# Performance work log

Measured on AMD Instinct MI355X. Metric: run time of the kernel, lower is better.

Reference implementation:

```python
import jax, jax.numpy as jnp
import numpy as np

N_NODES = 50000

def _gcn_conv(x, W, b, src, dst, num_nodes):
    # PyG GCNConv: linear transform, then D^{-1/2} A_hat D^{-1/2} aggregation (A_hat has self-loops).
    xw = x @ W                                   # [N, out]
    ones = jnp.ones(src.shape[0], dtype=x.dtype)
    deg = jax.ops.segment_sum(ones, dst, num_segments=num_nodes)  # in-degree incl. self loop
    dinv = jnp.where(deg > 0, jax.lax.rsqrt(deg), 0.0)
    norm = dinv[src] * dinv[dst]                 # [E]
    msg = xw[src] * norm[:, None]                # [E, out] gather + scale
    out = jax.ops.segment_sum(msg, dst, num_segments=num_nodes)   # scatter-add
    return out + b

def _add_self_loops(edge_index, num_nodes):
    loop = jnp.arange(num_nodes, dtype=edge_index.dtype)
    src = jnp.concatenate([edge_index[0], loop])
    dst = jnp.concatenate([edge_index[1], loop])
    return src, dst

def setup_inputs() -> dict:
    key = jax.random.key(0)
    k = jax.random.split(key, 6)
    in_dim, hid_dim, out_dim = 256, 128, 64
    n_edges = 800000
    x = jax.random.normal(k[0], (N_NODES, in_dim), dtype=jnp.float32)
    edge_index = jax.random.randint(k[1], (2, n_edges), 0, N_NODES, dtype=jnp.int64)
    W1 = jax.random.normal(k[2], (in_dim, hid_dim), dtype=jnp.float32) / np.sqrt(in_dim)
    b1 = jnp.zeros((hid_dim,), dtype=jnp.float32)
    W2 = jax.random.normal(k[3], (hid_dim, out_dim), dtype=jnp.float32) / np.sqrt(hid_dim)
    b2 = jnp.zeros((out_dim,), dtype=jnp.float32)
    return {"x": x, "edge_index": edge_index, "W1": W1, "b1": b1, "W2": W2, "b2": b2}

def reference(x, edge_index, W1, b1, W2, b2):
    src, dst = _add_self_loops(edge_index, N_NODES)
    h = jnp.tanh(_gcn_conv(x, W1, b1, src, dst, N_NODES))
    out = _gcn_conv(h, W2, b2, src, dst, N_NODES)
    return out
```

## Files before the change

### kernel.cpp

```cpp
#include <hip/hip_runtime.h>

#define INDIM 256
#define HID 128
#define OUTD 64
#define BINSHIFT 8
#define MAXBIN 256

typedef _Float16 f16x8 __attribute__((ext_vector_type(8)));
typedef float    f32x4 __attribute__((ext_vector_type(4)));

__global__ __launch_bounds__(256) void k_hist_setup(const int* __restrict__ dst, int* __restrict__ bin_counts,
                                                    int E,
                                                    const float* __restrict__ W1, const float* __restrict__ W2,
                                                    _Float16* __restrict__ W1t, _Float16* __restrict__ W2t) {
    __shared__ int h[MAXBIN];
    int tid = threadIdx.x;
    h[tid] = 0;
    __syncthreads();
    int base = blockIdx.x * 4096;
#pragma unroll
    for (int i = 0; i < 16; i++) {
        int e = base + i * 256 + tid;
        if (e < E) atomicAdd(&h[dst[e] >> BINSHIFT], 1);
    }
    __syncthreads();
    int v = h[tid];
    if (v) atomicAdd(&bin_counts[tid], v);

    constexpr int NW1 = HID * INDIM;
    constexpr int NW2 = OUTD * HID;
    int id = blockIdx.x * 256 + tid;
    if (id < NW1) {
        int n = id / INDIM, k = id % INDIM;
        W1t[id] = (_Float16)W1[k * HID + n];
    } else if (id < NW1 + NW2) {
        int j = id - NW1;
        int n = j / HID, k = j % HID;
        W2t[j] = (_Float16)W2[k * OUTD + n];
    }
}

struct __align__(16) GemmSh { _Float16 As[128][40]; _Float16 Bs[128][40]; };
struct FillSh { int h[256]; int s[256]; int rb[256]; };
struct CsrSh  { int A[256]; int B[256]; int C[256]; };
union FillU { FillSh f; GemmSh g; };
union CsrU  { CsrSh  c; GemmSh g; };

template <int BN, int K, typename AT>
__device__ __forceinline__ void gemm_body(const AT* __restrict__ X, const _Float16* __restrict__ Wt,
                                          _Float16* __restrict__ XW, int M, int rb,
                                          _Float16 (*As)[40], _Float16 (*Bs)[40])
{
    constexpr int NT = BN / 16;
    const int tid  = threadIdx.x;
    const int wave = tid >> 6;
    const int lane = tid & 63;
    const int m    = lane & 15;
    const int q    = lane >> 4;

    f32x4 acc[2][NT];
#pragma unroll
    for (int r = 0; r < 2; r++)
#pragma unroll
        for (int t = 0; t < NT; t++) acc[r][t] = (f32x4){0.f, 0.f, 0.f, 0.f};

    for (int kt = 0; kt < K; kt += 32) {
        if (kt) __syncthreads();
        if constexpr (sizeof(AT) == 4) {
#pragma unroll
            for (int i = 0; i < 4; i++) {
                int ch = tid + i * 256;
                int row = ch >> 3, c4 = ch & 7, gr = rb + row;
                float4 v = make_float4(0.f, 0.f, 0.f, 0.f);
                if (gr < M) v = *(const float4*)((const float*)X + (long)gr * K + kt + c4 * 4);
                _Float16* p = &As[row][c4 * 4];
                p[0] = (_Float16)v.x; p[1] = (_Float16)v.y;
                p[2] = (_Float16)v.z; p[3] = (_Float16)v.w;
            }
        } else {
#pragma unroll
            for (int i = 0; i < 2; i++) {
                int ch = tid + i * 256;
                int row = ch >> 2, c8 = ch & 3, gr = rb + row;
                uint4 v = make_uint4(0u, 0u, 0u, 0u);
                if (gr < M) v = *(const uint4*)((const _Float16*)X + (long)gr * K + kt + c8 * 8);
                *(uint4*)(&As[row][c8 * 8]) = v;
            }
        }
#pragma unroll
        for (int i = 0; i < BN / 64; i++) {
            int ch = tid + i * 256;
            int n = ch >> 2, c8 = ch & 3;
            *(uint4*)(&Bs[n][c8 * 8]) = *(const uint4*)(Wt + (long)n * K + kt + c8 * 8);
        }
        __syncthreads();

        f16x8 a0 = *(const f16x8*)(&As[wave * 32 + m][q * 8]);
        f16x8 a1 = *(const f16x8*)(&As[wave * 32 + 16 + m][q * 8]);
#pragma unroll
        for (int t = 0; t < NT; t++) {
            f16x8 bf = *(const f16x8*)(&Bs[t * 16 + m][q * 8]);
            acc[0][t] = __builtin_amdgcn_mfma_f32_16x16x32_f16(a0, bf, acc[0][t], 0, 0, 0);
            acc[1][t] = __builtin_amdgcn_mfma_f32_16x16x32_f16(a1, bf, acc[1][t], 0, 0, 0);
        }
    }

#pragma unroll
    for (int r2 = 0; r2 < 2; r2++) {
        int row0 = rb + wave * 32 + r2 * 16 + q * 4;
#pragma unroll
        for (int rr = 0; rr < 4; rr++) {
            int row = row0 + rr;
            if (row < M) {
#pragma unroll
                for (int t = 0; t < NT; t++)
                    XW[(long)row * BN + t * 16 + m] = (_Float16)acc[r2][t][rr];
            }
        }
    }
}

__device__ __forceinline__ void fill_body(const int* __restrict__ src, const int* __restrict__ dst,
                                          const int* __restrict__ bin_counts, int* __restrict__ bin_cursor,
                                          int* __restrict__ binned, int E, FillSh& sh)
{
    int tid = threadIdx.x;
    sh.h[tid] = 0;
    int v = bin_counts[tid];
    sh.s[tid] = v;
    __syncthreads();
    int base = blockIdx.x * 2048;
    int ep[8], eb[8], rk[8];
#pragma unroll
    for (int i = 0; i < 8; i++) {
        int e = base + i * 256 + tid;
        if (e < E) {
            int s = src[e], d = dst[e];
            ep[i] = (s << 8) | (d & 255);
            eb[i] = d >> BINSHIFT;
            rk[i] = atomicAdd(&sh.h[eb[i]], 1);
        } else {
            eb[i] = -1;
        }
    }
#pragma unroll
    for (int off = 1; off < 256; off <<= 1) {
        int t = (tid >= off) ? sh.s[tid - off] : 0;
        __syncthreads();
        sh.s[tid] += t;
        __syncthreads();
    }
    int c = sh.h[tid];
    if (c) sh.rb[tid] = (sh.s[tid] - v) + atomicAdd(&bin_cursor[tid], c);
    __syncthreads();
#pragma unroll
    for (int i = 0; i < 8; i++) {
        if (eb[i] >= 0) binned[sh.rb[eb[i]] + rk[i]] = ep[i];
    }
}

__device__ __forceinline__ void csr_body(const int* __restrict__ binned, const int* __restrict__ bin_counts,
                                         int* __restrict__ row_start, float* __restrict__ dinv,
                                         int* __restrict__ edge_src, int M, int E, CsrSh& sh)
{
    int b = blockIdx.x, tid = threadIdx.x;
    int v = bin_counts[tid];
    sh.A[tid] = v;
    __syncthreads();
#pragma unroll
    for (int off = 1; off < 256; off <<= 1) {
        int t = (tid >= off) ? sh.A[tid - off] : 0;
        __syncthreads();
        sh.A[tid] += t;
        __syncthreads();
    }
    sh.B[tid] = sh.A[tid] - v;
    __syncthreads();
    int beg = sh.B[b];
    int end = (b + 1 < 256) ? sh.B[b + 1] : E;
    if (b == 0 && tid == 0) row_start[M] = E;

    sh.A[tid] = 0;
    __syncthreads();
    for (int i = beg + tid; i < end; i += 256) {
        atomicAdd(&sh.A[binned[i] & 255], 1);
    }
    __syncthreads();
    int c = sh.A[tid];
    sh.B[tid] = c;
    __syncthreads();
#pragma unroll
    for (int off = 1; off < 256; off <<= 1) {
        int t = (tid >= off) ? sh.B[tid - off] : 0;
        __syncthreads();
        sh.B[tid] += t;
        __syncthreads();
    }
    int start = beg + sh.B[tid] - c;
    int node = (b << BINSHIFT) + tid;
    if (node < M) {
        row_start[node] = start;
        dinv[node] = rsqrtf(1.0f + (float)c);
    }
    sh.C[tid] = start;
    __syncthreads();
    for (int i = beg + tid; i < end; i += 256) {
        int p = binned[i];
        int pos = atomicAdd(&sh.C[p & 255], 1);
        edge_src[pos] = p >> 8;
    }
}

__global__ __launch_bounds__(256) void k_binfill_gemm(
    const int* __restrict__ src, const int* __restrict__ dst,
    const int* __restrict__ bin_counts, int* __restrict__ bin_cursor, int* __restrict__ binned, int E,
    const float* __restrict__ X, const _Float16* __restrict__ W1t, _Float16* __restrict__ XW, int M,
    int nfill, int rbofs)
{
    __shared__ FillU u;
    if ((int)blockIdx.x < nfill)
        fill_body(src, dst, bin_counts, bin_cursor, binned, E, u.f);
    else
        gemm_body<HID, INDIM, float>(X, W1t, XW, M, (rbofs + (int)blockIdx.x - nfill) * 128, u.g.As, u.g.Bs);
}

__global__ __launch_bounds__(256) void k_csr_gemm(
    const int* __restrict__ binned, const int* __restrict__ bin_counts,
    int* __restrict__ row_start, float* __restrict__ dinv, int* __restrict__ edge_src, int M, int E,
    const float* __restrict__ X, const _Float16* __restrict__ W1t, _Float16* __restrict__ XW,
    int nbin, int rbofs)
{
    __shared__ CsrU u;
    if ((int)blockIdx.x < nbin)
        csr_body(binned, bin_counts, row_start, dinv, edge_src, M, E, u.c);
    else
        gemm_body<HID, INDIM, float>(X, W1t, XW, M, (rbofs + (int)blockIdx.x - nbin) * 128, u.g.As, u.g.Bs);
}

template <int BN, int K, typename AT>
__global__ __launch_bounds__(256) void k_gemm_mfma(const AT* __restrict__ X, const _Float16* __restrict__ Wt,
                                                   _Float16* __restrict__ XW, int M)
{
    __shared__ __align__(16) _Float16 As[128][40];
    __shared__ __align__(16) _Float16 Bs[BN][40];
    gemm_body<BN, K, AT>(X, Wt, XW, M, (int)blockIdx.x * 128, As, Bs);
}

template <int F, bool TANH, typename OutT>
__global__ __launch_bounds__(256) void k_agg_csr(const int* __restrict__ row_start,
                                                 const int* __restrict__ edge_src,
                                                 const _Float16* __restrict__ feat,
                                                 const float* __restrict__ bias,
                                                 const float* __restrict__ dinv,
                                                 OutT* __restrict__ out, int M) {
    constexpr int LPN = F / 8;
    constexpr int NPB = 256 / LPN;
    int n = blockIdx.x * NPB + threadIdx.x / LPN;
    int c = threadIdx.x % LPN;
    if (n >= M) return;
    int beg = row_start[n], end = row_start[n + 1];
    float di = dinv[n];

    f16x8 self = *(const f16x8*)(feat + (long)n * F + c * 8);
    float acc[8], acc2[8];
#pragma unroll
    for (int k = 0; k < 8; k++) { acc[k] = di * (float)self[k]; acc2[k] = 0.f; }

    int j = beg;
    for (; j + 7 < end; j += 8) {
        int s0 = edge_src[j],     s1 = edge_src[j + 1];
        int s2 = edge_src[j + 2], s3 = edge_src[j + 3];
        int s4 = edge_src[j + 4], s5 = edge_src[j + 5];
        int s6 = edge_src[j + 6], s7 = edge_src[j + 7];
        float d0 = dinv[s0], d1 = dinv[s1], d2 = dinv[s2], d3 = dinv[s3];
        float d4 = dinv[s4], d5 = dinv[s5], d6 = dinv[s6], d7 = dinv[s7];
        f16x8 v0 = *(const f16x8*)(feat + (long)s0 * F + c * 8);
        f16x8 v1 = *(const f16x8*)(feat + (long)s1 * F + c * 8);
        f16x8 v2 = *(const f16x8*)(feat + (long)s2 * F + c * 8);
        f16x8 v3 = *(const f16x8*)(feat + (long)s3 * F + c * 8);
        f16x8 v4 = *(const f16x8*)(feat + (long)s4 * F + c * 8);
        f16x8 v5 = *(const f16x8*)(feat + (long)s5 * F + c * 8);
        f16x8 v6 = *(const f16x8*)(feat + (long)s6 * F + c * 8);
        f16x8 v7 = *(const f16x8*)(feat + (long)s7 * F + c * 8);
#pragma unroll
        for (int k = 0; k < 8; k++) {
            acc[k]  = fmaf(d0, (float)v0[k], acc[k]);
            acc2[k] = fmaf(d1, (float)v1[k], acc2[k]);
            acc[k]  = fmaf(d2, (float)v2[k], acc[k]);
            acc2[k] = fmaf(d3, (float)v3[k], acc2[k]);
            acc[k]  = fmaf(d4, (float)v4[k], acc[k]);
            acc2[k] = fmaf(d5, (float)v5[k], acc2[k]);
            acc[k]  = fmaf(d6, (float)v6[k], acc[k]);
            acc2[k] = fmaf(d7, (float)v7[k], acc2[k]);
        }
    }
    for (; j + 3 < end; j += 4) {
        int s0 = edge_src[j],     s1 = edge_src[j + 1];
        int s2 = edge_src[j + 2], s3 = edge_src[j + 3];
        float d0 = dinv[s0], d1 = dinv[s1], d2 = dinv[s2], d3 = dinv[s3];
        f16x8 v0 = *(const f16x8*)(feat + (long)s0 * F + c * 8);
        f16x8 v1 = *(const f16x8*)(feat + (long)s1 * F + c * 8);
        f16x8 v2 = *(const f16x8*)(feat + (long)s2 * F + c * 8);
        f16x8 v3 = *(const f16x8*)(feat + (long)s3 * F + c * 8);
#pragma unroll
        for (int k = 0; k < 8; k++) {
            acc[k]  = fmaf(d0, (float)v0[k], acc[k]);
            acc2[k] = fmaf(d1, (float)v1[k], acc2[k]);
            acc[k]  = fmaf(d2, (float)v2[k], acc[k]);
            acc2[k] = fmaf(d3, (float)v3[k], acc2[k]);
        }
    }
    for (; j < end; j++) {
        int s = edge_src[j];
        float d = dinv[s];
        f16x8 v = *(const f16x8*)(feat + (long)s * F + c * 8);
#pragma unroll
        for (int k = 0; k < 8; k++) acc[k] = fmaf(d, (float)v[k], acc[k]);
    }

    float r[8];
#pragma unroll
    for (int k = 0; k < 8; k++) r[k] = bias[c * 8 + k] + di * (acc[k] + acc2[k]);
    if (TANH) {
#pragma unroll
        for (int k = 0; k < 8; k++) r[k] = tanhf(r[k]);
    }
    if constexpr (sizeof(OutT) == 2) {
        f16x8 o;
#pragma unroll
        for (int k = 0; k < 8; k++) o[k] = (_Float16)r[k];
        __builtin_nontemporal_store(o, (f16x8*)((_Float16*)out + (long)n * F + c * 8));
    } else {
        f32x4 o0 = {r[0], r[1], r[2], r[3]};
        f32x4 o1 = {r[4], r[5], r[6], r[7]};
        float* p = (float*)out + (long)n * F + c * 8;
        __builtin_nontemporal_store(o0, (f32x4*)p);
        __builtin_nontemporal_store(o1, (f32x4*)(p + 4));
    }
}

extern "C" void kernel_launch(void* const* d_in, const int* in_sizes, int n_in,
                              void* d_out, int out_size, void* d_ws, size_t ws_size,
                              hipStream_t stream) {
    const float* x  = (const float*)d_in[0];
    const int*   ei = (const int*)d_in[1];
    const float* W1 = (const float*)d_in[2];
    const float* b1 = (const float*)d_in[3];
    const float* W2 = (const float*)d_in[4];
    const float* b2 = (const float*)d_in[5];
    float* out = (float*)d_out;

    const int M = in_sizes[0] / INDIM;
    const int E = in_sizes[1] / 2;
    const int* srcp = ei;
    const int* dstp = ei + E;

    const int Mp   = (M + 63) & ~63;
    const int NBIN = (M + 255) >> BINSHIFT;

    float*     dinv       = (float*)d_ws;
    int*       row_start  = (int*)(dinv + Mp);
    int*       bin_cursor = row_start + Mp;
    int*       bin_counts = bin_cursor + MAXBIN;
    _Float16*  W1t        = (_Float16*)(bin_counts + MAXBIN);
    _Float16*  W2t        = W1t + HID * INDIM;
    int*       binned     = (int*)(W2t + OUTD * HID);
    int*       edge_src   = binned + E;
    _Float16*  xw16       = (_Float16*)(edge_src + E);
    _Float16*  h16        = xw16 + (long)M * HID;
    _Float16*  hw16       = xw16;

    const int NWH = (E + 4095) / 4096;
    const int NWF = (E + 2047) / 2048;
    const int GB  = (M + 127) / 128;
    const int GA  = GB / 3;
    const int GBc = GB - GA;

    hipMemsetAsync(bin_cursor, 0, 2 * MAXBIN * sizeof(int), stream);
    k_hist_setup<<<NWH, 256, 0, stream>>>(dstp, bin_counts, E, W1, W2, W1t, W2t);
    k_binfill_gemm<<<NWF + GA, 256, 0, stream>>>(srcp, dstp, bin_counts, bin_cursor, binned, E,
                                                 x, W1t, xw16, M, NWF, 0);
    k_csr_gemm<<<NBIN + GBc, 256, 0, stream>>>(binned, bin_counts, row_start, dinv, edge_src, M, E,
                                               x, W1t, xw16, NBIN, GA);

    k_agg_csr<HID, true, _Float16><<<(M + 15) / 16, 256, 0, stream>>>(row_start, edge_src, xw16, b1, dinv, h16, M);

    k_gemm_mfma<OUTD, HID, _Float16><<<GB, 256, 0, stream>>>(h16, W2t, hw16, M);
    k_agg_csr<OUTD, false, float><<<(M + 31) / 32, 256, 0, stream>>>(row_start, edge_src, hw16, b2, dinv, out, M);
}
```

Measured before the change: 222.0 us.

## Fuse layer-1 aggregation with layer-2 GEMM and pre-scale by dinv

Layer-1 aggregation now writes its tanh output to shared memory, and the same block immediately multiplies those 16 rows by W2 with MFMA. This removes the round trip of h16 through global memory and one kernel launch. The GEMM output is pre-scaled by the source node's dinv, so layer-2 aggregation can drop the per-edge dinv gathers and use plain adds. The cost is that each block's MFMA tile covers only 16 rows, and W2 is reread from global memory by every block.

```diff
diff --git a/kernel.cpp b/kernel.cpp
--- a/kernel.cpp
+++ b/kernel.cpp
@@ -237,34 +237,139 @@
         gemm_body<HID, INDIM, float>(X, W1t, XW, M, (rbofs + (int)blockIdx.x - nbin) * 128, u.g.As, u.g.Bs);
 }
 
-template <int BN, int K, typename AT>
-__global__ __launch_bounds__(256) void k_gemm_mfma(const AT* __restrict__ X, const _Float16* __restrict__ Wt,
-                                                   _Float16* __restrict__ XW, int M)
-{
-    __shared__ __align__(16) _Float16 As[128][40];
-    __shared__ __align__(16) _Float16 Bs[BN][40];
-    gemm_body<BN, K, AT>(X, Wt, XW, M, (int)blockIdx.x * 128, As, Bs);
-}
-
-template <int F, bool TANH, typename OutT>
-__global__ __launch_bounds__(256) void k_agg_csr(const int* __restrict__ row_start,
-                                                 const int* __restrict__ edge_src,
-                                                 const _Float16* __restrict__ feat,
-                                                 const float* __restrict__ bias,
-                                                 const float* __restrict__ dinv,
-                                                 OutT* __restrict__ out, int M) {
+__global__ __launch_bounds__(256) void k_agg1_gemm2(
+    const int* __restrict__ row_start, const int* __restrict__ edge_src,
+    const _Float16* __restrict__ feat,
+    const float* __restrict__ bias,
+    const float* __restrict__ dinv,
+    const _Float16* __restrict__ W2t,
+    _Float16* __restrict__ hw16, int M)
+{
+    constexpr int F = HID;
+    __shared__ __align__(16) _Float16 Hs[16][136];
+    __shared__ float Ds[16];
+
+    const int tid = threadIdx.x;
+    const int nl  = tid >> 4;
+    const int c   = tid & 15;
+    const int n   = blockIdx.x * 16 + nl;
+
+    float r[8];
+    float di = 0.f;
+    if (n < M) {
+        di = dinv[n];
+        int beg = row_start[n], end = row_start[n + 1];
+        f16x8 self = *(const f16x8*)(feat + (long)n * F + c * 8);
+        float acc[8], acc2[8];
+#pragma unroll
+        for (int k = 0; k < 8; k++) { acc[k] = di * (float)self[k]; acc2[k] = 0.f; }
+
+        int j = beg;
+        for (; j + 7 < end; j += 8) {
+            int s0 = edge_src[j],     s1 = edge_src[j + 1];
+            int s2 = edge_src[j + 2], s3 = edge_src[j + 3];
+            int s4 = edge_src[j + 4], s5 = edge_src[j + 5];
+            int s6 = edge_src[j + 6], s7 = edge_src[j + 7];
+            float d0 = dinv[s0], d1 = dinv[s1], d2 = dinv[s2], d3 = dinv[s3];
+            float d4 = dinv[s4], d5 = dinv[s5], d6 = dinv[s6], d7 = dinv[s7];
+            f16x8 v0 = *(const f16x8*)(feat + (long)s0 * F + c * 8);
+            f16x8 v1 = *(const f16x8*)(feat + (long)s1 * F + c * 8);
+            f16x8 v2 = *(const f16x8*)(feat + (long)s2 * F + c * 8);
+            f16x8 v3 = *(const f16x8*)(feat + (long)s3 * F + c * 8);
+            f16x8 v4 = *(const f16x8*)(feat + (long)s4 * F + c * 8);
+            f16x8 v5 = *(const f16x8*)(feat + (long)s5 * F + c * 8);
+            f16x8 v6 = *(const f16x8*)(feat + (long)s6 * F + c * 8);
+            f16x8 v7 = *(const f16x8*)(feat + (long)s7 * F + c * 8);
+#pragma unroll
+            for (int k = 0; k < 8; k++) {
+                acc[k]  = fmaf(d0, (float)v0[k], acc[k]);
+                acc2[k] = fmaf(d1, (float)v1[k], acc2[k]);
+                acc[k]  = fmaf(d2, (float)v2[k], acc[k]);
+                acc2[k] = fmaf(d3, (float)v3[k], acc2[k]);
+                acc[k]  = fmaf(d4, (float)v4[k], acc[k]);
+                acc2[k] = fmaf(d5, (float)v5[k], acc2[k]);
+                acc[k]  = fmaf(d6, (float)v6[k], acc[k]);
+                acc2[k] = fmaf(d7, (float)v7[k], acc2[k]);
+            }
+        }
+        for (; j + 3 < end; j += 4) {
+            int s0 = edge_src[j],     s1 = edge_src[j + 1];
+            int s2 = edge_src[j + 2], s3 = edge_src[j + 3];
+            float d0 = dinv[s0], d1 = dinv[s1], d2 = dinv[s2], d3 = dinv[s3];
+            f16x8 v0 = *(const f16x8*)(feat + (long)s0 * F + c * 8);
+            f16x8 v1 = *(const f16x8*)(feat + (long)s1 * F + c * 8);
+            f16x8 v2 = *(const f16x8*)(feat + (long)s2 * F + c * 8);
+            f16x8 v3 = *(const f16x8*)(feat + (long)s3 * F + c * 8);
+#pragma unroll
+            for (int k = 0; k < 8; k++) {
+                acc[k]  = fmaf(d0, (float)v0[k], acc[k]);
+                acc2[k] = fmaf(d1, (float)v1[k], acc2[k]);
+                acc[k]  = fmaf(d2, (float)v2[k], acc[k]);
+                acc2[k] = fmaf(d3, (float)v3[k], acc2[k]);
+            }
+        }
+        for (; j < end; j++) {
+            int s = edge_src[j];
+            float d = dinv[s];
+            f16x8 v = *(const f16x8*)(feat + (long)s * F + c * 8);
+#pragma unroll
+            for (int k = 0; k < 8; k++) acc[k] = fmaf(d, (float)v[k], acc[k]);
+        }
+
+#pragma unroll
+        for (int k = 0; k < 8; k++) r[k] = tanhf(bias[c * 8 + k] + di * (acc[k] + acc2[k]));
+    } else {
+#pragma unroll
+        for (int k = 0; k < 8; k++) r[k] = 0.f;
+    }
+
+    f16x8 hh;
+#pragma unroll
+    for (int k = 0; k < 8; k++) hh[k] = (_Float16)r[k];
+    *(f16x8*)(&Hs[nl][c * 8]) = hh;
+    if (c == 0) Ds[nl] = di;
+    __syncthreads();
+
+    const int wave = tid >> 6;
+    const int lane = tid & 63;
+    const int m    = lane & 15;
+    const int q    = lane >> 4;
+    const _Float16* Wb = W2t + (long)(wave * 16 + m) * HID;
+
+    f32x4 acc = (f32x4){0.f, 0.f, 0.f, 0.f};
+#pragma unroll
+    for (int kt = 0; kt < HID; kt += 32) {
+        f16x8 af = *(const f16x8*)(&Hs[m][kt + q * 8]);
+        f16x8 bf = *(const f16x8*)(Wb + kt + q * 8);
+        acc = __builtin_amdgcn_mfma_f32_16x16x32_f16(af, bf, acc, 0, 0, 0);
+    }
+#pragma unroll
+    for (int rr = 0; rr < 4; rr++) {
+        int nl2 = q * 4 + rr;
+        int row = blockIdx.x * 16 + nl2;
+        if (row < M)
+            hw16[(long)row * OUTD + wave * 16 + m] = (_Float16)(acc[rr] * Ds[nl2]);
+    }
+}
+
+template <int F>
+__global__ __launch_bounds__(256) void k_agg2(const int* __restrict__ row_start,
+                                              const int* __restrict__ edge_src,
+                                              const _Float16* __restrict__ feat,
+                                              const float* __restrict__ bias,
+                                              const float* __restrict__ dinv,
+                                              float* __restrict__ out, int M) {
     constexpr int LPN = F / 8;
     constexpr int NPB = 256 / LPN;
     int n = blockIdx.x * NPB + threadIdx.x / LPN;
     int c = threadIdx.x % LPN;
     if (n >= M) return;
     int beg = row_start[n], end = row_start[n + 1];
-    float di = dinv[n];
 
     f16x8 self = *(const f16x8*)(feat + (long)n * F + c * 8);
     float acc[8], acc2[8];
 #pragma unroll
-    for (int k = 0; k < 8; k++) { acc[k] = di * (float)self[k]; acc2[k] = 0.f; }
+    for (int k = 0; k < 8; k++) { acc[k] = (float)self[k]; acc2[k] = 0.f; }
 
     int j = beg;
     for (; j + 7 < end; j += 8) {
@@ -272,8 +377,6 @@
         int s2 = edge_src[j + 2], s3 = edge_src[j + 3];
         int s4 = edge_src[j + 4], s5 = edge_src[j + 5];
         int s6 = edge_src[j + 6], s7 = edge_src[j + 7];
-        float d0 = dinv[s0], d1 = dinv[s1], d2 = dinv[s2], d3 = dinv[s3];
-        float d4 = dinv[s4], d5 = dinv[s5], d6 = dinv[s6], d7 = dinv[s7];
         f16x8 v0 = *(const f16x8*)(feat + (long)s0 * F + c * 8);
         f16x8 v1 = *(const f16x8*)(feat + (long)s1 * F + c * 8);
         f16x8 v2 = *(const f16x8*)(feat + (long)s2 * F + c * 8);
@@ -284,59 +387,41 @@
         f16x8 v7 = *(const f16x8*)(feat + (long)s7 * F + c * 8);
 #pragma unroll
         for (int k = 0; k < 8; k++) {
-            acc[k]  = fmaf(d0, (float)v0[k], acc[k]);
-            acc2[k] = fmaf(d1, (float)v1[k], acc2[k]);
-            acc[k]  = fmaf(d2, (float)v2[k], acc[k]);
-            acc2[k] = fmaf(d3, (float)v3[k], acc2[k]);
-            acc[k]  = fmaf(d4, (float)v4[k], acc[k]);
-            acc2[k] = fmaf(d5, (float)v5[k], acc2[k]);
-            acc[k]  = fmaf(d6, (float)v6[k], acc[k]);
-            acc2[k] = fmaf(d7, (float)v7[k], acc2[k]);
+            acc[k]  += (float)v0[k] + (float)v1[k];
+            acc2[k] += (float)v2[k] + (float)v3[k];
+            acc[k]  += (float)v4[k] + (float)v5[k];
+            acc2[k] += (float)v6[k] + (float)v7[k];
         }
     }
     for (; j + 3 < end; j += 4) {
         int s0 = edge_src[j],     s1 = edge_src[j + 1];
         int s2 = edge_src[j + 2], s3 = edge_src[j + 3];
-        float d0 = dinv[s0], d1 = dinv[s1], d2 = dinv[s2], d3 = dinv[s3];
         f16x8 v0 = *(const f16x8*)(feat + (long)s0 * F + c * 8);
         f16x8 v1 = *(const f16x8*)(feat + (long)s1 * F + c * 8);
         f16x8 v2 = *(const f16x8*)(feat + (long)s2 * F + c * 8);
         f16x8 v3 = *(const f16x8*)(feat + (long)s3 * F + c * 8);
 #pragma unroll
         for (int k = 0; k < 8; k++) {
-            acc[k]  = fmaf(d0, (float)v0[k], acc[k]);
-            acc2[k] = fmaf(d1, (float)v1[k], acc2[k]);
-            acc[k]  = fmaf(d2, (float)v2[k], acc[k]);
-            acc2[k] = fmaf(d3, (float)v3[k], acc2[k]);
+            acc[k]  += (float)v0[k] + (float)v1[k];
+            acc2[k] += (float)v2[k] + (float)v3[k];
         }
     }
     for (; j < end; j++) {
         int s = edge_src[j];
-        float d = dinv[s];
         f16x8 v = *(const f16x8*)(feat + (long)s * F + c * 8);
 #pragma unroll
-        for (int k = 0; k < 8; k++) acc[k] = fmaf(d, (float)v[k], acc[k]);
-    }
-
+        for (int k = 0; k < 8; k++) acc[k] += (float)v[k];
+    }
+
+    float di = dinv[n];
     float r[8];
 #pragma unroll
     for (int k = 0; k < 8; k++) r[k] = bias[c * 8 + k] + di * (acc[k] + acc2[k]);
-    if (TANH) {
-#pragma unroll
-        for (int k = 0; k < 8; k++) r[k] = tanhf(r[k]);
-    }
-    if constexpr (sizeof(OutT) == 2) {
-        f16x8 o;
-#pragma unroll
-        for (int k = 0; k < 8; k++) o[k] = (_Float16)r[k];
-        __builtin_nontemporal_store(o, (f16x8*)((_Float16*)out + (long)n * F + c * 8));
-    } else {
-        f32x4 o0 = {r[0], r[1], r[2], r[3]};
-        f32x4 o1 = {r[4], r[5], r[6], r[7]};
-        float* p = (float*)out + (long)n * F + c * 8;
-        __builtin_nontemporal_store(o0, (f32x4*)p);
-        __builtin_nontemporal_store(o1, (f32x4*)(p + 4));
-    }
+    f32x4 o0 = {r[0], r[1], r[2], r[3]};
+    f32x4 o1 = {r[4], r[5], r[6], r[7]};
+    float* p = out + (long)n * F + c * 8;
+    __builtin_nontemporal_store(o0, (f32x4*)p);
+    __builtin_nontemporal_store(o1, (f32x4*)(p + 4));
 }
 
 extern "C" void kernel_launch(void* const* d_in, const int* in_sizes, int n_in,
@@ -367,8 +452,7 @@
     int*       binned     = (int*)(W2t + OUTD * HID);
     int*       edge_src   = binned + E;
     _Float16*  xw16       = (_Float16*)(edge_src + E);
-    _Float16*  h16        = xw16 + (long)M * HID;
-    _Float16*  hw16       = xw16;
+    _Float16*  hw16       = xw16 + (long)M * HID;
 
     const int NWH = (E + 4095) / 4096;
     const int NWF = (E + 2047) / 2048;
@@ -383,8 +467,7 @@
     k_csr_gemm<<<NBIN + GBc, 256, 0, stream>>>(binned, bin_counts, row_start, dinv, edge_src, M, E,
                                                x, W1t, xw16, NBIN, GA);
 
-    k_agg_csr<HID, true, _Float16><<<(M + 15) / 16, 256, 0, stream>>>(row_start, edge_src, xw16, b1, dinv, h16, M);
-
-    k_gemm_mfma<OUTD, HID, _Float16><<<GB, 256, 0, stream>>>(h16, W2t, hw16, M);
-    k_agg_csr<OUTD, false, float><<<(M + 31) / 32, 256, 0, stream>>>(row_start, edge_src, hw16, b2, dinv, out, M);
-}
+    k_agg1_gemm2<<<(M + 15) / 16, 256, 0, stream>>>(row_start, edge_src, xw16, b1, dinv, W2t, hw16, M);
+
+    k_agg2<OUTD><<<(M + 31) / 32, 256, 0, stream>>>(row_start, edge_src, hw16, b2, dinv, out, M);
+}
```

After: 224.1 us. No clear change (+1.0%).

## Split aggregation by feature chunks and prescale layer-2 GEMM output by dinv

Applied to the files above, without the earlier changes.

The two aggregation kernels now map blocks to feature chunks: each block handles a 16-wide (layer 1) or 8-wide (layer 2) slice for 128 or 256 nodes. This narrows the gathered working set per pass so it stays cache-resident, at the cost of re-reading the CSR indices once per chunk. The layer-2 GEMM epilogue multiplies each row by dinv, so the second aggregation can drop the per-edge dinv gather and do plain sums. The layer-2 projected features now get their own buffer instead of reusing xw16.

```diff
diff --git a/kernel.cpp b/kernel.cpp
--- a/kernel.cpp
+++ b/kernel.cpp
@@ -48,6 +48,7 @@
 
 template <int BN, int K, typename AT>
 __device__ __forceinline__ void gemm_body(const AT* __restrict__ X, const _Float16* __restrict__ Wt,
+                                          const float* __restrict__ dscale,
                                           _Float16* __restrict__ XW, int M, int rb,
                                           _Float16 (*As)[40], _Float16 (*Bs)[40])
 {
@@ -112,9 +113,10 @@
         for (int rr = 0; rr < 4; rr++) {
             int row = row0 + rr;
             if (row < M) {
+                float sc = dscale ? dscale[row] : 1.f;
 #pragma unroll
                 for (int t = 0; t < NT; t++)
-                    XW[(long)row * BN + t * 16 + m] = (_Float16)acc[r2][t][rr];
+                    XW[(long)row * BN + t * 16 + m] = (_Float16)(acc[r2][t][rr] * sc);
             }
         }
     }
@@ -221,7 +223,7 @@
     if ((int)blockIdx.x < nfill)
         fill_body(src, dst, bin_counts, bin_cursor, binned, E, u.f);
     else
-        gemm_body<HID, INDIM, float>(X, W1t, XW, M, (rbofs + (int)blockIdx.x - nfill) * 128, u.g.As, u.g.Bs);
+        gemm_body<HID, INDIM, float>(X, W1t, nullptr, XW, M, (rbofs + (int)blockIdx.x - nfill) * 128, u.g.As, u.g.Bs);
 }
 
 __global__ __launch_bounds__(256) void k_csr_gemm(
@@ -234,34 +236,34 @@
     if ((int)blockIdx.x < nbin)
         csr_body(binned, bin_counts, row_start, dinv, edge_src, M, E, u.c);
     else
-        gemm_body<HID, INDIM, float>(X, W1t, XW, M, (rbofs + (int)blockIdx.x - nbin) * 128, u.g.As, u.g.Bs);
+        gemm_body<HID, INDIM, float>(X, W1t, nullptr, XW, M, (rbofs + (int)blockIdx.x - nbin) * 128, u.g.As, u.g.Bs);
 }
 
 template <int BN, int K, typename AT>
 __global__ __launch_bounds__(256) void k_gemm_mfma(const AT* __restrict__ X, const _Float16* __restrict__ Wt,
+                                                   const float* __restrict__ dscale,
                                                    _Float16* __restrict__ XW, int M)
 {
     __shared__ __align__(16) _Float16 As[128][40];
     __shared__ __align__(16) _Float16 Bs[BN][40];
-    gemm_body<BN, K, AT>(X, Wt, XW, M, (int)blockIdx.x * 128, As, Bs);
-}
-
-template <int F, bool TANH, typename OutT>
-__global__ __launch_bounds__(256) void k_agg_csr(const int* __restrict__ row_start,
-                                                 const int* __restrict__ edge_src,
-                                                 const _Float16* __restrict__ feat,
-                                                 const float* __restrict__ bias,
-                                                 const float* __restrict__ dinv,
-                                                 OutT* __restrict__ out, int M) {
-    constexpr int LPN = F / 8;
-    constexpr int NPB = 256 / LPN;
-    int n = blockIdx.x * NPB + threadIdx.x / LPN;
-    int c = threadIdx.x % LPN;
+    gemm_body<BN, K, AT>(X, Wt, dscale, XW, M, (int)blockIdx.x * 128, As, Bs);
+}
+
+__global__ __launch_bounds__(256) void k_agg1(
+    const int* __restrict__ row_start, const int* __restrict__ edge_src,
+    const _Float16* __restrict__ feat,
+    const float* __restrict__ bias,
+    const float* __restrict__ dinv,
+    _Float16* __restrict__ h16, int M)
+{
+    const int chunk = blockIdx.x & 7;
+    const int n = ((int)blockIdx.x >> 3) * 128 + ((int)threadIdx.x >> 1);
     if (n >= M) return;
+    const int fo = chunk * 16 + (threadIdx.x & 1) * 8;
+
+    float di = dinv[n];
     int beg = row_start[n], end = row_start[n + 1];
-    float di = dinv[n];
-
-    f16x8 self = *(const f16x8*)(feat + (long)n * F + c * 8);
+    f16x8 self = *(const f16x8*)(feat + (long)n * HID + fo);
     float acc[8], acc2[8];
 #pragma unroll
     for (int k = 0; k < 8; k++) { acc[k] = di * (float)self[k]; acc2[k] = 0.f; }
@@ -274,14 +276,14 @@
         int s6 = edge_src[j + 6], s7 = edge_src[j + 7];
         float d0 = dinv[s0], d1 = dinv[s1], d2 = dinv[s2], d3 = dinv[s3];
         float d4 = dinv[s4], d5 = dinv[s5], d6 = dinv[s6], d7 = dinv[s7];
-        f16x8 v0 = *(const f16x8*)(feat + (long)s0 * F + c * 8);
-        f16x8 v1 = *(const f16x8*)(feat + (long)s1 * F + c * 8);
-        f16x8 v2 = *(const f16x8*)(feat + (long)s2 * F + c * 8);
-        f16x8 v3 = *(const f16x8*)(feat + (long)s3 * F + c * 8);
-        f16x8 v4 = *(const f16x8*)(feat + (long)s4 * F + c * 8);
-        f16x8 v5 = *(const f16x8*)(feat + (long)s5 * F + c * 8);
-        f16x8 v6 = *(const f16x8*)(feat + (long)s6 * F + c * 8);
-        f16x8 v7 = *(const f16x8*)(feat + (long)s7 * F + c * 8);
+        f16x8 v0 = *(const f16x8*)(feat + (long)s0 * HID + fo);
+        f16x8 v1 = *(const f16x8*)(feat + (long)s1 * HID + fo);
+        f16x8 v2 = *(const f16x8*)(feat + (long)s2 * HID + fo);
+        f16x8 v3 = *(const f16x8*)(feat + (long)s3 * HID + fo);
+        f16x8 v4 = *(const f16x8*)(feat + (long)s4 * HID + fo);
+        f16x8 v5 = *(const f16x8*)(feat + (long)s5 * HID + fo);
+        f16x8 v6 = *(const f16x8*)(feat + (long)s6 * HID + fo);
+        f16x8 v7 = *(const f16x8*)(feat + (long)s7 * HID + fo);
 #pragma unroll
         for (int k = 0; k < 8; k++) {
             acc[k]  = fmaf(d0, (float)v0[k], acc[k]);
@@ -298,10 +300,10 @@
         int s0 = edge_src[j],     s1 = edge_src[j + 1];
         int s2 = edge_src[j + 2], s3 = edge_src[j + 3];
         float d0 = dinv[s0], d1 = dinv[s1], d2 = dinv[s2], d3 = dinv[s3];
-        f16x8 v0 = *(const f16x8*)(feat + (long)s0 * F + c * 8);
-        f16x8 v1 = *(const f16x8*)(feat + (long)s1 * F + c * 8);
-        f16x8 v2 = *(const f16x8*)(feat + (long)s2 * F + c * 8);
-        f16x8 v3 = *(const f16x8*)(feat + (long)s3 * F + c * 8);
+        f16x8 v0 = *(const f16x8*)(feat + (long)s0 * HID + fo);
+        f16x8 v1 = *(const f16x8*)(feat + (long)s1 * HID + fo);
+        f16x8 v2 = *(const f16x8*)(feat + (long)s2 * HID + fo);
+        f16x8 v3 = *(const f16x8*)(feat + (long)s3 * HID + fo);
 #pragma unroll
         for (int k = 0; k < 8; k++) {
             acc[k]  = fmaf(d0, (float)v0[k], acc[k]);
@@ -313,30 +315,87 @@
     for (; j < end; j++) {
         int s = edge_src[j];
         float d = dinv[s];
-        f16x8 v = *(const f16x8*)(feat + (long)s * F + c * 8);
+        f16x8 v = *(const f16x8*)(feat + (long)s * HID + fo);
 #pragma unroll
         for (int k = 0; k < 8; k++) acc[k] = fmaf(d, (float)v[k], acc[k]);
     }
 
+    f16x8 hh;
+#pragma unroll
+    for (int k = 0; k < 8; k++)
+        hh[k] = (_Float16)tanhf(bias[fo + k] + di * (acc[k] + acc2[k]));
+    *(f16x8*)(h16 + (long)n * HID + fo) = hh;
+}
+
+__global__ __launch_bounds__(256) void k_agg2(
+    const int* __restrict__ row_start, const int* __restrict__ edge_src,
+    const _Float16* __restrict__ feat,
+    const float* __restrict__ bias,
+    const float* __restrict__ dinv,
+    float* __restrict__ out, int M)
+{
+    const int chunk = blockIdx.x & 7;
+    const int n = ((int)blockIdx.x >> 3) * 256 + (int)threadIdx.x;
+    if (n >= M) return;
+    const int fo = chunk * 8;
+
+    int beg = row_start[n], end = row_start[n + 1];
+    f16x8 self = *(const f16x8*)(feat + (long)n * OUTD + fo);
+    float acc[8], acc2[8];
+#pragma unroll
+    for (int k = 0; k < 8; k++) { acc[k] = (float)self[k]; acc2[k] = 0.f; }
+
+    int j = beg;
+    for (; j + 7 < end; j += 8) {
+        int s0 = edge_src[j],     s1 = edge_src[j + 1];
+        int s2 = edge_src[j + 2], s3 = edge_src[j + 3];
+        int s4 = edge_src[j + 4], s5 = edge_src[j + 5];
+        int s6 = edge_src[j + 6], s7 = edge_src[j + 7];
+        f16x8 v0 = *(const f16x8*)(feat + (long)s0 * OUTD + fo);
+        f16x8 v1 = *(const f16x8*)(feat + (long)s1 * OUTD + fo);
+        f16x8 v2 = *(const f16x8*)(feat + (long)s2 * OUTD + fo);
+        f16x8 v3 = *(const f16x8*)(feat + (long)s3 * OUTD + fo);
+        f16x8 v4 = *(const f16x8*)(feat + (long)s4 * OUTD + fo);
+        f16x8 v5 = *(const f16x8*)(feat + (long)s5 * OUTD + fo);
+        f16x8 v6 = *(const f16x8*)(feat + (long)s6 * OUTD + fo);
+        f16x8 v7 = *(const f16x8*)(feat + (long)s7 * OUTD + fo);
+#pragma unroll
+        for (int k = 0; k < 8; k++) {
+            acc[k]  += (float)v0[k] + (float)v1[k];
+            acc2[k] += (float)v2[k] + (float)v3[k];
+            acc[k]  += (float)v4[k] + (float)v5[k];
+            acc2[k] += (float)v6[k] + (float)v7[k];
+        }
+    }
+    for (; j + 3 < end; j += 4) {
+        int s0 = edge_src[j],     s1 = edge_src[j + 1];
+        int s2 = edge_src[j + 2], s3 = edge_src[j + 3];
+        f16x8 v0 = *(const f16x8*)(feat + (long)s0 * OUTD + fo);
+        f16x8 v1 = *(const f16x8*)(feat + (long)s1 * OUTD + fo);
+        f16x8 v2 = *(const f16x8*)(feat + (long)s2 * OUTD + fo);
+        f16x8 v3 = *(const f16x8*)(feat + (long)s3 * OUTD + fo);
+#pragma unroll
+        for (int k = 0; k < 8; k++) {
+            acc[k]  += (float)v0[k] + (float)v1[k];
+            acc2[k] += (float)v2[k] + (float)v3[k];
+        }
+    }
+    for (; j < end; j++) {
+        int s = edge_src[j];
+        f16x8 v = *(const f16x8*)(feat + (long)s * OUTD + fo);
+#pragma unroll
+        for (int k = 0; k < 8; k++) acc[k] += (float)v[k];
+    }
+
+    float di = dinv[n];
     float r[8];
 #pragma unroll
-    for (int k = 0; k < 8; k++) r[k] = bias[c * 8 + k] + di * (acc[k] + acc2[k]);
-    if (TANH) {
-#pragma unroll
-        for (int k = 0; k < 8; k++) r[k] = tanhf(r[k]);
-    }
-    if constexpr (sizeof(OutT) == 2) {
-        f16x8 o;
-#pragma unroll
-        for (int k = 0; k < 8; k++) o[k] = (_Float16)r[k];
-        __builtin_nontemporal_store(o, (f16x8*)((_Float16*)out + (long)n * F + c * 8));
-    } else {
-        f32x4 o0 = {r[0], r[1], r[2], r[3]};
-        f32x4 o1 = {r[4], r[5], r[6], r[7]};
-        float* p = (float*)out + (long)n * F + c * 8;
-        __builtin_nontemporal_store(o0, (f32x4*)p);
-        __builtin_nontemporal_store(o1, (f32x4*)(p + 4));
-    }
+    for (int k = 0; k < 8; k++) r[k] = bias[fo + k] + di * (acc[k] + acc2[k]);
+    f32x4 o0 = {r[0], r[1], r[2], r[3]};
+    f32x4 o1 = {r[4], r[5], r[6], r[7]};
+    float* p = out + (long)n * OUTD + fo;
+    __builtin_nontemporal_store(o0, (f32x4*)p);
+    __builtin_nontemporal_store(o1, (f32x4*)(p + 4));
 }
 
 extern "C" void kernel_launch(void* const* d_in, const int* in_sizes, int n_in,
@@ -368,7 +427,7 @@
     int*       edge_src   = binned + E;
     _Float16*  xw16       = (_Float16*)(edge_src + E);
     _Float16*  h16        = xw16 + (long)M * HID;
-    _Float16*  hw16       = xw16;
+    _Float16*  hw16       = h16 + (long)M * HID;
 
     const int NWH = (E + 4095) / 4096;
     const int NWF = (E + 2047) / 2048;
@@ -383,8 +442,9 @@
     k_csr_gemm<<<NBIN + GBc, 256, 0, stream>>>(binned, bin_counts, row_start, dinv, edge_src, M, E,
                                                x, W1t, xw16, NBIN, GA);
 
-    k_agg_csr<HID, true, _Float16><<<(M + 15) / 16, 256, 0, stream>>>(row_start, edge_src, xw16, b1, dinv, h16, M);
-
-    k_gemm_mfma<OUTD, HID, _Float16><<<GB, 256, 0, stream>>>(h16, W2t, hw16, M);
-    k_agg_csr<OUTD, false, float><<<(M + 31) / 32, 256, 0, stream>>>(row_start, edge_src, hw16, b2, dinv, out, M);
-}
+    k_agg1<<<((M + 127) / 128) * 8, 256, 0, stream>>>(row_start, edge_src, xw16, b1, dinv, h16, M);
+
+    k_gemm_mfma<OUTD, HID, _Float16><<<GB, 256, 0, stream>>>(h16, W2t, dinv, hw16, M);
+
+    k_agg2<<<((M + 255) / 256) * 8, 256, 0, stream>>>(row_start, edge_src, hw16, b2, dinv, out, M);
+}
```

Result: slower. 340.4 us (+53.3%).
